# Kernel optimization log

Hardware: AMD Instinct MI355X
Metric: run time of the kernel (lower is better)

Reference implementation:

```python
import jax, jax.numpy as jnp
import numpy as np
from jax import lax

BS, H, W, NA = 128, 64, 64, 4
C1, C2, HID = 16, 32, 512

def setup_inputs() -> dict:
    key = jax.random.key(0)
    ks = jax.random.split(key, 12)
    s = 0.05
    return {
        "diffs": jax.random.uniform(ks[0], (BS, NA, 2), jnp.float32) * 4.0,  # agent locations
        "states": jax.random.normal(ks[1], (BS, NA * 3, H, W), jnp.float32),
        "conv1_w": jax.random.normal(ks[2], (C1, 3, 8, 8), jnp.float32) * s,
        "conv1_b": jnp.zeros((C1,), jnp.float32),
        "conv2_w": jax.random.normal(ks[3], (C2, C1, 5, 5), jnp.float32) * s,
        "conv2_b": jnp.zeros((C2,), jnp.float32),
        "g_w": jax.random.normal(ks[4], (HID, 2 * C2 + 2), jnp.float32) * s,
        "g_b": jnp.zeros((HID,), jnp.float32),
        "fc4_w": jax.random.normal(ks[5], (2, HID), jnp.float32) * s,
        "fc4_b": jnp.zeros((2,), jnp.float32),
        "fc5_w": jax.random.normal(ks[6], (1, HID), jnp.float32) * s,
        "fc5_b": jnp.zeros((1,), jnp.float32),
    }

def _conv(x, w, b):
    y = lax.conv_general_dilated(x, w, (1, 1), 'VALID',
                                 dimension_numbers=('NCHW', 'OIHW', 'NCHW'))
    return jax.nn.relu(y + b[None, :, None, None])

def reference(diffs, states, conv1_w, conv1_b, conv2_w, conv2_b,
              g_w, g_b, fc4_w, fc4_b, fc5_w, fc5_b):
    bs = states.shape[0]
    # ---- encoder: per-agent CNN + global max pool ----
    x = states.reshape(bs * NA, 3, H, W)
    x = _conv(x, conv1_w, conv1_b)
    x = _conv(x, conv2_w, conv2_b)
    feat = jnp.max(x, axis=(2, 3)).reshape(bs, NA, C2)  # (bs, 4, 32)
    # ---- coordinator: adjacency from pairwise location diffs ----
    locs = diffs
    pdiffs = locs[:, :, None, :] - locs[:, None, :, :]  # (bs, 4, 4, 2)
    norms = jnp.linalg.norm(pdiffs, axis=-1)
    thresh = jnp.linalg.norm(jnp.array([1.0, 1.0], jnp.float32))
    A = (norms < thresh).astype(jnp.float32)
    A = A / jnp.clip(jnp.sum(A, axis=-1, keepdims=True), 1e-6)  # row-normalized adjacency
    mask = 1.0 - jnp.eye(NA, dtype=jnp.float32)  # messages skip j == i
    Am = A * mask  # (bs, 4, 4)
    # ---- CatEdgeGraphLayer: h_i = relu(W [f_i ; sum_j A_ij [f_j ; d_ij]] + b) ----
    feat_agg = jnp.einsum('bij,bjc->bic', Am, feat)          # (bs, 4, 32)
    diff_agg = jnp.einsum('bij,bijd->bid', Am, pdiffs)       # (bs, 4, 2)
    h = jnp.concatenate([feat, feat_agg, diff_agg], axis=-1)  # (bs, 4, 66)
    h = jax.nn.relu(jnp.einsum('bic,oc->bio', h, g_w) + g_b)  # (bs, 4, 512)
    policies = jnp.einsum('bic,oc->bio', h, fc4_w) + fc4_b    # (bs, 4, 2)
    values = jnp.einsum('bic,oc->bio', h, fc5_w) + fc5_b      # (bs, 4, 1)
    return (policies, values)
```

## Files before the change

kernel.cpp:

```cpp
#include <hip/hip_runtime.h>
#include <hip/hip_bf16.h>

#define H1 57
#define H2 53
#define XP 60

typedef _Float16 f16;
typedef _Float16 f16x4 __attribute__((ext_vector_type(4)));
typedef _Float16 f16x8 __attribute__((ext_vector_type(8)));
typedef float f32x4 __attribute__((ext_vector_type(4)));
typedef float f32x16 __attribute__((ext_vector_type(16)));

__global__ __launch_bounds__(256) void k_repack(const float* __restrict__ w1,
    const float* __restrict__ w2, const float* __restrict__ gw,
    f16* __restrict__ w1f, f16* __restrict__ w2f,
    float2* __restrict__ gwT2, float* __restrict__ feat)
{
  const int tid = blockIdx.x * 256 + threadIdx.x;
  const int stride = 32 * 256;
  for (int i = tid; i < 8 * 64 * 8; i += stride) {
    int j = i & 7;
    int l = (i >> 3) & 63;
    int tp = i >> 9;
    int c = j & 3;
    int kw = 2 * (l >> 4) + (j >> 2);
    int oc = l & 15;
    float v = (c < 3) ? w1[((oc * 3 + c) * 8 + tp) * 8 + kw] : 0.f;
    w1f[i] = (f16)v;
  }
  for (int i = tid; i < 25 * 64 * 8; i += stride) {
    int j = i & 7;
    int l = (i >> 3) & 63;
    int tap = i >> 9;
    int oc = l & 31;
    int ch = ((l >> 5) << 3) + j;
    w2f[i] = (f16)w2[((oc * 16 + ch) * 5 + tap / 5) * 5 + tap % 5];
  }
  for (int i = tid; i < 66 * 256; i += stride) {
    int t = i & 255;
    int c = i >> 8;
    float2 v;
    v.x = gw[(2 * t) * 66 + c];
    v.y = gw[(2 * t + 1) * 66 + c];
    gwT2[i] = v;
  }
  for (int i = tid; i < 512 * 32; i += stride) feat[i] = 0.f;
}

__global__ __launch_bounds__(256) void k_conv1(const float* __restrict__ in,
    const f16* __restrict__ w1f, const float* __restrict__ b1,
    f16* __restrict__ O1)
{
  __shared__ __align__(16) f16 sIn[15][72][4];
  __shared__ __align__(16) f16 sT[4][64][20];
  const int img = blockIdx.x;
  const int y0 = min((int)blockIdx.y * 8, 49);
  const int lane = threadIdx.x & 63;
  const int wv = threadIdx.x >> 6;

  f16x8 Bf[8];
  #pragma unroll
  for (int tp = 0; tp < 8; ++tp)
    Bf[tp] = *(const f16x8*)&w1f[(tp * 64 + lane) * 8];

  for (int i = threadIdx.x; i < 15 * 16; i += 256) {
    int y = i >> 4, xq = i & 15;
    const float* p0 = &in[(((size_t)img * 3 + 0) * 64 + (y0 + y)) * 64 + xq * 4];
    float4 v0 = *(const float4*)p0;
    float4 v1 = *(const float4*)(p0 + 4096);
    float4 v2 = *(const float4*)(p0 + 8192);
    float c0[4] = {v0.x, v0.y, v0.z, v0.w};
    float c1[4] = {v1.x, v1.y, v1.z, v1.w};
    float c2[4] = {v2.x, v2.y, v2.z, v2.w};
    #pragma unroll
    for (int q = 0; q < 4; ++q) {
      f16x4 tt = {(f16)c0[q], (f16)c1[q], (f16)c2[q], (f16)0.f};
      *(f16x4*)&sIn[y][xq * 4 + q][0] = tt;
    }
  }
  for (int i = threadIdx.x; i < 15 * 8; i += 256) {
    int y = i >> 3, xi = i & 7;
    *(f16x4*)&sIn[y][64 + xi][0] = (f16x4){(f16)0.f, (f16)0.f, (f16)0.f, (f16)0.f};
  }
  __syncthreads();

  const int g = lane >> 4;
  const int n16 = lane & 15;

  const float bias = b1[n16];
  f32x4 acc[2][4];
  #pragma unroll
  for (int r = 0; r < 2; ++r)
    #pragma unroll
    for (int xt = 0; xt < 4; ++xt)
      acc[r][xt] = (f32x4){bias, bias, bias, bias};

  #pragma unroll
  for (int tp = 0; tp < 8; ++tp) {
    #pragma unroll
    for (int r = 0; r < 2; ++r) {
      const int row = 2 * wv + r + tp;
      #pragma unroll
      for (int xt = 0; xt < 4; ++xt) {
        const int px = xt * 16 + n16;
        f16x4 a0 = *(const f16x4*)&sIn[row][px + 2 * g][0];
        f16x4 a1 = *(const f16x4*)&sIn[row][px + 2 * g + 1][0];
        union { struct { f16x4 lo, hi; } pr; f16x8 v; } u;
        u.pr.lo = a0; u.pr.hi = a1;
        acc[r][xt] = __builtin_amdgcn_mfma_f32_16x16x32_f16(u.v, Bf[tp], acc[r][xt], 0, 0, 0);
      }
    }
  }

  #pragma unroll
  for (int r = 0; r < 2; ++r) {
    #pragma unroll
    for (int xt = 0; xt < 4; ++xt)
      #pragma unroll
      for (int q = 0; q < 4; ++q)
        sT[wv][xt * 16 + g * 4 + q][n16] = (f16)fmaxf(acc[r][xt][q], 0.f);
    const int yy = y0 + 2 * wv + r;
    if (lane < H1) {
      f16x4 v0 = *(const f16x4*)&sT[wv][lane][0];
      f16x4 v1 = *(const f16x4*)&sT[wv][lane][4];
      f16x4 v2 = *(const f16x4*)&sT[wv][lane][8];
      f16x4 v3 = *(const f16x4*)&sT[wv][lane][12];
      union { struct { f16x4 a, b; } pr; f16x8 v; } lo, hi;
      lo.pr.a = v0; lo.pr.b = v1;
      hi.pr.a = v2; hi.pr.b = v3;
      f16* dst = &O1[(((size_t)img * H1 + yy) * XP + lane) * 16];
      *(f16x8*)dst = lo.v;
      *(f16x8*)(dst + 8) = hi.v;
    }
  }
}

__global__ __launch_bounds__(256, 4) void k_conv2(const f16* __restrict__ O1,
    const f16* __restrict__ w2f, const float* __restrict__ b2,
    float* __restrict__ feat)
{
  __shared__ __align__(16) f16 sW[17 * 64 * 8];
  __shared__ __align__(16) f16 sI[12 * 2 * 60 * 8 + 64];
  __shared__ unsigned smax[32];
  const int img = blockIdx.x;
  const int y0 = min((int)blockIdx.y * 8, 45);
  const int lane = threadIdx.x & 63;
  const int wv = threadIdx.x >> 6;
  if (threadIdx.x < 32) smax[threadIdx.x] = 0u;

  f16x8 Br[8];
  const f16* pBg = &w2f[lane * 8];
  #pragma unroll
  for (int t = 0; t < 8; ++t)
    Br[t] = *(const f16x8*)(pBg + t * 512);

  for (int i = threadIdx.x; i < 17 * 64; i += 256)
    ((float4*)sW)[i] = ((const float4*)w2f)[8 * 64 + i];
  for (int i = threadIdx.x; i < 1440; i += 256) {
    int y = i / 120;
    int rem = i - y * 120;
    int oct = rem / 60;
    int x = rem - oct * 60;
    ((float4*)sI)[i] =
        *(const float4*)(O1 + (((size_t)img * H1 + y0 + y) * XP + x) * 16 + oct * 8);
  }
  __syncthreads();

  const int m32 = lane & 31;
  const int G = lane >> 5;

  const float bias = b2[m32];
  f32x16 acc[2][2];
  #pragma unroll
  for (int r = 0; r < 2; ++r)
    #pragma unroll
    for (int h = 0; h < 2; ++h)
      #pragma unroll
      for (int q = 0; q < 16; ++q)
        acc[r][h][q] = bias;

  const f16* pA[2][2];
  #pragma unroll
  for (int r = 0; r < 2; ++r)
    #pragma unroll
    for (int h = 0; h < 2; ++h)
      pA[r][h] = &sI[(((2 * wv + r) * 2 + G) * XP + h * 32 + m32) * 8];
  const f16* pB = &sW[lane * 8];

  #pragma unroll
  for (int tap = 0; tap < 25; ++tap) {
    const int kh = tap / 5, kw = tap % 5;
    const int off = (kh * 2 * XP + kw) * 8;
    f16x8 Bv = (tap < 8) ? Br[tap] : *(const f16x8*)(pB + (tap - 8) * 512);
    #pragma unroll
    for (int r = 0; r < 2; ++r)
      #pragma unroll
      for (int h = 0; h < 2; ++h) {
        f16x8 Av = *(const f16x8*)(pA[r][h] + off);
        acc[r][h] = __builtin_amdgcn_mfma_f32_32x32x16_f16(Av, Bv, acc[r][h], 0, 0, 0);
      }
  }

  float m = 0.f;
  #pragma unroll
  for (int r = 0; r < 2; ++r)
    #pragma unroll
    for (int h = 0; h < 2; ++h)
      #pragma unroll
      for (int q = 0; q < 16; ++q) {
        int row = (q & 3) + 8 * (q >> 2) + 4 * G;
        int px = h * 32 + row;
        if (px < H2) m = fmaxf(m, acc[r][h][q]);
      }
  m = fmaxf(m, 0.f);
  m = fmaxf(m, __shfl_xor(m, 32, 64));
  if (lane < 32) atomicMax(&smax[m32], __float_as_uint(m));
  __syncthreads();
  if (threadIdx.x < 32)
    atomicMax((unsigned*)&feat[img * 32 + threadIdx.x], smax[threadIdx.x]);
}

__global__ __launch_bounds__(256) void k_head(const float* __restrict__ diffs,
    const float* __restrict__ feat, const float2* __restrict__ gwT2,
    const float* __restrict__ gb, const float* __restrict__ w4,
    const float* __restrict__ b4, const float* __restrict__ w5,
    const float* __restrict__ b5, float* __restrict__ out)
{
  __shared__ float h66[4][66];
  __shared__ float hout[4][512];
  __shared__ float Am[4][4];
  __shared__ float pd[4][4][2];
  __shared__ float fs[4][32];
  const int b = blockIdx.x;
  const int tid = threadIdx.x;
  if (tid < 128) {
    int i = tid >> 5, c = tid & 31;
    fs[i][c] = feat[(b * 4 + i) * 32 + c];
  }
  if (tid == 0) {
    float lx[4], ly[4];
    #pragma unroll
    for (int a = 0; a < 4; ++a) {
      lx[a] = diffs[(b * 4 + a) * 2];
      ly[a] = diffs[(b * 4 + a) * 2 + 1];
    }
    #pragma unroll
    for (int i = 0; i < 4; ++i) {
      float A[4];
      float rs = 0.f;
      #pragma unroll
      for (int j = 0; j < 4; ++j) {
        float dx = lx[i] - lx[j], dy = ly[i] - ly[j];
        pd[i][j][0] = dx;
        pd[i][j][1] = dy;
        float n = sqrtf(dx * dx + dy * dy);
        A[j] = (n < 1.41421356237309504880f) ? 1.f : 0.f;
        rs += A[j];
      }
      float inv = 1.f / fmaxf(rs, 1e-6f);
      #pragma unroll
      for (int j = 0; j < 4; ++j)
        Am[i][j] = (i == j) ? 0.f : A[j] * inv;
    }
  }
  __syncthreads();
  if (tid < 128) {
    int i = tid >> 5, c = tid & 31;
    h66[i][c] = fs[i][c];
    float s = 0.f;
    #pragma unroll
    for (int j = 0; j < 4; ++j) s += Am[i][j] * fs[j][c];
    h66[i][32 + c] = s;
  } else if (tid < 136) {
    int q = tid - 128;
    int i = q >> 1, d = q & 1;
    float s = 0.f;
    #pragma unroll
    for (int j = 0; j < 4; ++j) s += Am[i][j] * pd[i][j][d];
    h66[i][64 + d] = s;
  }
  __syncthreads();
  {
    const float b0 = gb[2 * tid], b1g = gb[2 * tid + 1];
    float a[4][2];
    #pragma unroll
    for (int i = 0; i < 4; ++i) { a[i][0] = b0; a[i][1] = b1g; }
    #pragma unroll 6
    for (int c = 0; c < 66; ++c) {
      float2 w = gwT2[c * 256 + tid];
      #pragma unroll
      for (int i = 0; i < 4; ++i) {
        float h = h66[i][c];
        a[i][0] = fmaf(h, w.x, a[i][0]);
        a[i][1] = fmaf(h, w.y, a[i][1]);
      }
    }
    #pragma unroll
    for (int i = 0; i < 4; ++i) {
      float2 v;
      v.x = fmaxf(a[i][0], 0.f);
      v.y = fmaxf(a[i][1], 0.f);
      *(float2*)&hout[i][2 * tid] = v;
    }
  }
  __syncthreads();
  if (tid < 192) {
    int gq = tid >> 4, l = tid & 15;
    int i = gq / 3, k = gq % 3;
    const float* wrow = (k < 2) ? &w4[k * 512] : w5;
    float s = 0.f;
    for (int o = l; o < 512; o += 16) s = fmaf(hout[i][o], wrow[o], s);
    #pragma unroll
    for (int d = 8; d >= 1; d >>= 1) s += __shfl_xor(s, d, 16);
    if (l == 0) {
      if (k < 2) out[(b * 4 + i) * 2 + k] = s + b4[k];
      else       out[1024 + b * 4 + i] = s + b5[0];
    }
  }
}

extern "C" void kernel_launch(void* const* d_in, const int* in_sizes, int n_in,
                              void* d_out, int out_size, void* d_ws, size_t ws_size,
                              hipStream_t stream) {
  const float* diffs  = (const float*)d_in[0];
  const float* states = (const float*)d_in[1];
  const float* w1 = (const float*)d_in[2];
  const float* b1 = (const float*)d_in[3];
  const float* w2 = (const float*)d_in[4];
  const float* b2 = (const float*)d_in[5];
  const float* gw = (const float*)d_in[6];
  const float* gb = (const float*)d_in[7];
  const float* w4 = (const float*)d_in[8];
  const float* b4 = (const float*)d_in[9];
  const float* w5 = (const float*)d_in[10];
  const float* b5 = (const float*)d_in[11];
  float* out = (float*)d_out;

  char* base = (char*)d_ws;
  f16*    w1f  = (f16*)base;
  f16*    w2f  = (f16*)(base + 8192);
  float2* gwT2 = (float2*)(base + 34816);
  float*  feat = (float*)(base + 169984);
  f16*    O1   = (f16*)(base + 235520);

  k_repack<<<32, 256, 0, stream>>>(w1, w2, gw, w1f, w2f, gwT2, feat);
  k_conv1<<<dim3(512, 8), 256, 0, stream>>>(states, w1f, b1, O1);
  k_conv2<<<dim3(512, 7), 256, 0, stream>>>(O1, w2f, b2, feat);
  k_head<<<128, 256, 0, stream>>>(diffs, feat, gwT2, gb, w4, b4, w5, b5, out);
}
```

Measured before the change: 90.01 us.

## Pack conv2 output pixels densely into MFMA tiles and split-octet conv1 layout

Conv1 output is now stored with the two 8-channel octets in separate planes, so conv2 can copy its input slab contiguously. Conv2 no longer maps each output row onto two 32-pixel MFMA tiles, which wasted 11 of 64 columns per row. It flattens the 8x53 output pixels into 14 dense 32-pixel tiles spread unevenly over 4 waves (4,4,3,3). This removes wasted MFMA work but adds per-lane division indexing, clamped padding pixels and load imbalance between waves.

```diff
diff --git a/kernel.cpp b/kernel.cpp
--- a/kernel.cpp
+++ b/kernel.cpp
@@ -128,9 +128,9 @@
       union { struct { f16x4 a, b; } pr; f16x8 v; } lo, hi;
       lo.pr.a = v0; lo.pr.b = v1;
       hi.pr.a = v2; hi.pr.b = v3;
-      f16* dst = &O1[(((size_t)img * H1 + yy) * XP + lane) * 16];
+      f16* dst = &O1[((((size_t)img * H1 + yy) * 2 + 0) * XP + lane) * 8];
       *(f16x8*)dst = lo.v;
-      *(f16x8*)(dst + 8) = hi.v;
+      *(f16x8*)(dst + XP * 8) = hi.v;
     }
   }
 }
@@ -140,7 +140,7 @@
     float* __restrict__ feat)
 {
   __shared__ __align__(16) f16 sW[17 * 64 * 8];
-  __shared__ __align__(16) f16 sI[12 * 2 * 60 * 8 + 64];
+  __shared__ __align__(16) f16 sI[12 * 2 * XP * 8 + 64];
   __shared__ unsigned smax[32];
   const int img = blockIdx.x;
   const int y0 = min((int)blockIdx.y * 8, 45);
@@ -156,62 +156,64 @@
 
   for (int i = threadIdx.x; i < 17 * 64; i += 256)
     ((float4*)sW)[i] = ((const float4*)w2f)[8 * 64 + i];
-  for (int i = threadIdx.x; i < 1440; i += 256) {
-    int y = i / 120;
-    int rem = i - y * 120;
-    int oct = rem / 60;
-    int x = rem - oct * 60;
-    ((float4*)sI)[i] =
-        *(const float4*)(O1 + (((size_t)img * H1 + y0 + y) * XP + x) * 16 + oct * 8);
+  {
+    const float4* src = (const float4*)(O1 + (size_t)(img * H1 + y0) * (2 * XP * 8));
+    for (int i = threadIdx.x; i < 1440; i += 256)
+      ((float4*)sI)[i] = src[i];
   }
   __syncthreads();
 
   const int m32 = lane & 31;
   const int G = lane >> 5;
 
+  const int start = (wv < 2) ? wv * 4 : 8 + (wv - 2) * 3;
+  const int cnt = (wv < 2) ? 4 : 3;
+
   const float bias = b2[m32];
-  f32x16 acc[2][2];
-  #pragma unroll
-  for (int r = 0; r < 2; ++r)
-    #pragma unroll
-    for (int h = 0; h < 2; ++h)
-      #pragma unroll
-      for (int q = 0; q < 16; ++q)
-        acc[r][h][q] = bias;
-
-  const f16* pA[2][2];
-  #pragma unroll
-  for (int r = 0; r < 2; ++r)
-    #pragma unroll
-    for (int h = 0; h < 2; ++h)
-      pA[r][h] = &sI[(((2 * wv + r) * 2 + G) * XP + h * 32 + m32) * 8];
-  const f16* pB = &sW[lane * 8];
+  f32x16 acc[4];
+  #pragma unroll
+  for (int ti = 0; ti < 4; ++ti)
+    #pragma unroll
+    for (int q = 0; q < 16; ++q)
+      acc[ti][q] = bias;
+
+  const f16* pA[4];
+  #pragma unroll
+  for (int ti = 0; ti < 4; ++ti) {
+    int t = start + ti;
+    int p = t * 32 + m32;
+    p = min(p, 423);
+    int y = (p * 1237) >> 16;
+    int x = p - 53 * y;
+    pA[ti] = &sI[((y * 2 + G) * XP + x) * 8];
+  }
 
   #pragma unroll
   for (int tap = 0; tap < 25; ++tap) {
     const int kh = tap / 5, kw = tap % 5;
     const int off = (kh * 2 * XP + kw) * 8;
-    f16x8 Bv = (tap < 8) ? Br[tap] : *(const f16x8*)(pB + (tap - 8) * 512);
-    #pragma unroll
-    for (int r = 0; r < 2; ++r)
-      #pragma unroll
-      for (int h = 0; h < 2; ++h) {
-        f16x8 Av = *(const f16x8*)(pA[r][h] + off);
-        acc[r][h] = __builtin_amdgcn_mfma_f32_32x32x16_f16(Av, Bv, acc[r][h], 0, 0, 0);
-      }
+    f16x8 Bv = (tap < 8) ? Br[tap] : *(const f16x8*)(&sW[lane * 8] + (tap - 8) * 512);
+    #pragma unroll
+    for (int ti = 0; ti < 4; ++ti) {
+      if (ti < cnt) {
+        f16x8 Av = *(const f16x8*)(pA[ti] + off);
+        acc[ti] = __builtin_amdgcn_mfma_f32_32x32x16_f16(Av, Bv, acc[ti], 0, 0, 0);
+      }
+    }
   }
 
   float m = 0.f;
   #pragma unroll
-  for (int r = 0; r < 2; ++r)
-    #pragma unroll
-    for (int h = 0; h < 2; ++h)
+  for (int ti = 0; ti < 4; ++ti) {
+    if (ti < cnt) {
+      const int t = start + ti;
       #pragma unroll
       for (int q = 0; q < 16; ++q) {
-        int row = (q & 3) + 8 * (q >> 2) + 4 * G;
-        int px = h * 32 + row;
-        if (px < H2) m = fmaxf(m, acc[r][h][q]);
-      }
+        if (t == 13 && q >= 4) continue;
+        m = fmaxf(m, acc[ti][q]);
+      }
+    }
+  }
   m = fmaxf(m, 0.f);
   m = fmaxf(m, __shfl_xor(m, 32, 64));
   if (lane < 32) atomicMax(&smax[m32], __float_as_uint(m));
```

Result: faster. 88.22 us (-2.0%).
